# Optimization experiments

Measured on AMD Instinct MI355X. Metric: run time of the kernel, lower is better.

Reference implementation:

```python
import jax, jax.numpy as jnp
import numpy as np

N = 100000      # nodes
E = 1600000     # edges
F_IN = 256      # input feature dim
H = 2           # num heads
D = 64          # hidden per head (H*D = 128)
C = 64          # output classes
N_TRAIN = 10000
SLOPE = 0.2     # DGL GATConv leaky_relu negative slope
BN_EPS = 1e-5


def setup_inputs() -> dict:
    key = jax.random.key(0)
    ks = jax.random.split(key, 20)
    sc = lambda k, shape, fan: jax.random.normal(k, shape, jnp.float32) * np.float32(1.0 / np.sqrt(fan))
    inp = {}
    inp["feature"] = jax.random.normal(ks[0], (N, F_IN), jnp.float32)
    inp["label"] = jax.random.randint(ks[1], (N,), 0, C, dtype=jnp.int32)
    inp["train_nodes"] = jax.random.randint(ks[2], (N_TRAIN,), 0, N, dtype=jnp.int32)
    inp["src"] = jax.random.randint(ks[3], (E,), 0, N, dtype=jnp.int32)
    inp["dst"] = jax.random.randint(ks[4], (E,), 0, N, dtype=jnp.int32)
    # GATConv layer 0: F_IN -> H*D
    inp["W0"] = sc(ks[5], (F_IN, H * D), F_IN)
    inp["al0"] = sc(ks[6], (H, D), D)
    inp["ar0"] = sc(ks[7], (H, D), D)
    inp["b0"] = jnp.zeros((H * D,), jnp.float32)
    # GATConv layer 1: H*D -> H*D
    inp["W1"] = sc(ks[8], (H * D, H * D), H * D)
    inp["al1"] = sc(ks[9], (H, D), D)
    inp["ar1"] = sc(ks[10], (H, D), D)
    inp["b1"] = jnp.zeros((H * D,), jnp.float32)
    # dense head: Linear(H*D -> D) + ReLU, Linear(D -> C), BatchNorm1d(C)
    inp["Wout"] = sc(ks[11], (H * D, D), H * D)
    inp["bout"] = jnp.zeros((D,), jnp.float32)
    inp["Wfc"] = sc(ks[12], (D, C), D)
    inp["bfc"] = jnp.zeros((C,), jnp.float32)
    inp["gamma"] = jnp.ones((C,), jnp.float32)
    inp["beta"] = jnp.zeros((C,), jnp.float32)
    return inp


def gat_conv(x, W, al, ar, b, src, dst):
    """DGL-style GATConv: gather, edge attention, segment softmax over dst, scatter-sum, ReLU."""
    n = x.shape[0]
    feat = (x @ W).reshape(n, H, D)                      # [N,H,D]
    el = jnp.einsum('nhd,hd->nh', feat, al)              # src attention term
    er = jnp.einsum('nhd,hd->nh', feat, ar)              # dst attention term
    e = jax.nn.leaky_relu(el[src] + er[dst], SLOPE)      # [E,H]
    m = jax.ops.segment_max(e, dst, num_segments=n)      # per-dst max for stable softmax
    exp_e = jnp.exp(e - m[dst])
    denom = jax.ops.segment_sum(exp_e, dst, num_segments=n)
    alpha = exp_e / jnp.maximum(denom[dst], 1e-16)       # [E,H]
    msg = feat[src] * alpha[:, :, None]                  # [E,H,D]
    out = jax.ops.segment_sum(msg, dst, num_segments=n)  # [N,H,D]
    out = out + b.reshape(1, H, D)
    return jax.nn.relu(out)


def reference(feature, label, train_nodes, src, dst,
              W0, al0, ar0, b0, W1, al1, ar1, b1,
              Wout, bout, Wfc, bfc, gamma, beta):
    h = gat_conv(feature, W0, al0, ar0, b0, src, dst).reshape(N, H * D)
    h = gat_conv(h, W1, al1, ar1, b1, src, dst).reshape(N, H * D)
    h = jax.nn.relu(h @ Wout + bout)
    h = h @ Wfc + bfc
    # BatchNorm1d in training mode: batch statistics (biased variance)
    mu = jnp.mean(h, axis=0)
    var = jnp.mean((h - mu) ** 2, axis=0)
    h = (h - mu) * jax.lax.rsqrt(var + BN_EPS) * gamma + beta
    p = jax.nn.softmax(h, axis=1)
    # F.cross_entropy applied to softmax outputs, exactly as in the source
    sel = p[train_nodes]                                  # [N_TRAIN, C]
    logp = jax.nn.log_softmax(sel, axis=1)
    lab = label[train_nodes]
    loss = -jnp.mean(jnp.take_along_axis(logp, lab[:, None], axis=1))
    return (p, loss)
```

## Files before the change

kernel.cpp:

```cpp
#include <hip/hip_runtime.h>

#define SLOPE 0.2f
#define BN_EPS 1e-5f

#define CSR_TILE 4096
#define NBUCK_SH 9
#define BCAP 16384

typedef __attribute__((ext_vector_type(8))) short bf16x8;
typedef __attribute__((ext_vector_type(4))) float f32x4;

__device__ __forceinline__ float wave_sum(float v){
  #pragma unroll
  for(int o=32;o;o>>=1) v += __shfl_xor(v,o);
  return v;
}
__device__ __forceinline__ float wave_max(float v){
  #pragma unroll
  for(int o=32;o;o>>=1) v = fmaxf(v,__shfl_xor(v,o));
  return v;
}
__device__ __forceinline__ unsigned pack_bf16(float a, float b){
  unsigned ua=__float_as_uint(a), ub=__float_as_uint(b);
  ua += 0x7fffu + ((ua>>16)&1u);
  ub += 0x7fffu + ((ub>>16)&1u);
  return (ua>>16) | (ub & 0xffff0000u);
}
__device__ __forceinline__ float bf_lo(unsigned u){ return __uint_as_float(u<<16); }
__device__ __forceinline__ float bf_hi(unsigned u){ return __uint_as_float(u & 0xffff0000u); }

__global__ __launch_bounds__(256) void wtrans2(const float* __restrict__ W0,
    const float* __restrict__ W1, unsigned* __restrict__ Wt0, unsigned* __restrict__ Wt1){
  int idx = blockIdx.x*256 + threadIdx.x;
  if(blockIdx.x < 64){
    int c = idx >> 7, kp = idx & 127;
    Wt0[(size_t)c*128 + kp] = pack_bf16(W0[(size_t)(2*kp)*128 + c], W0[(size_t)(2*kp+1)*128 + c]);
  } else {
    int i2 = idx - 64*256;
    int c = i2 >> 6, kp = i2 & 63;
    Wt1[(size_t)c*64 + kp] = pack_bf16(W1[(size_t)(2*kp)*128 + c], W1[(size_t)(2*kp+1)*128 + c]);
  }
}

template<int AF32>
__global__ __launch_bounds__(256) void gemm_mfma(const void* __restrict__ Aptr,
    const unsigned* __restrict__ Wt, unsigned* __restrict__ outb,
    const float* __restrict__ al, const float* __restrict__ ar,
    float* __restrict__ el, float* __restrict__ er, int n, int K){
  __shared__ unsigned sA[128][36];
  int t = threadIdx.x;
  int w = t >> 6, l = t & 63;
  int wr = (w >> 1) * 64, wc = (w & 1) * 64;
  int row0 = blockIdx.x * 128;
  int K2 = K >> 1;
  int ktiles = K >> 6;

  int srow[4], sslot[4];
  #pragma unroll
  for(int i=0;i<4;i++){ int u4 = t + i*256; srow[i] = u4>>3; sslot[i] = u4&7; }

  uint4 pa[4][2];

  auto load_tile = [&](int kt){
    if(AF32){
      const float* A = (const float*)Aptr;
      #pragma unroll
      for(int i=0;i<4;i++){
        int gr = row0 + srow[i];
        pa[i][0] = make_uint4(0,0,0,0);
        pa[i][1] = make_uint4(0,0,0,0);
        if(gr < n){
          const unsigned* ap = (const unsigned*)(A + (size_t)gr*K + kt*64 + sslot[i]*8);
          pa[i][0] = *(const uint4*)ap;
          pa[i][1] = *(const uint4*)(ap+4);
        }
      }
    } else {
      const unsigned* A = (const unsigned*)Aptr;
      #pragma unroll
      for(int i=0;i<4;i++){
        int gr = row0 + srow[i];
        pa[i][0] = make_uint4(0,0,0,0);
        if(gr < n) pa[i][0] = *(const uint4*)(A + (size_t)gr*K2 + kt*32 + sslot[i]*4);
      }
    }
  };

  auto store_tile = [&](){
    if(AF32){
      #pragma unroll
      for(int i=0;i<4;i++){
        uint4 v;
        v.x = pack_bf16(__uint_as_float(pa[i][0].x), __uint_as_float(pa[i][0].y));
        v.y = pack_bf16(__uint_as_float(pa[i][0].z), __uint_as_float(pa[i][0].w));
        v.z = pack_bf16(__uint_as_float(pa[i][1].x), __uint_as_float(pa[i][1].y));
        v.w = pack_bf16(__uint_as_float(pa[i][1].z), __uint_as_float(pa[i][1].w));
        *(uint4*)&sA[srow[i]][sslot[i]*4] = v;
      }
    } else {
      #pragma unroll
      for(int i=0;i<4;i++)
        *(uint4*)&sA[srow[i]][sslot[i]*4] = pa[i][0];
    }
  };

  f32x4 zero4 = {0.f,0.f,0.f,0.f};
  f32x4 acc[4][4];
  #pragma unroll
  for(int i=0;i<4;i++)
    #pragma unroll
    for(int j=0;j<4;j++) acc[i][j] = zero4;

  int rl = l & 15;
  load_tile(0);
  for(int kt = 0; kt < ktiles; ++kt){
    store_tile();
    __syncthreads();
    if(kt+1 < ktiles) load_tile(kt+1);
    #pragma unroll
    for(int ks=0; ks<2; ++ks){
      int koff = ks*16 + (l>>4)*4;
      bf16x8 a[4], b[4];
      #pragma unroll
      for(int f=0; f<4; f++)
        b[f] = *(const bf16x8*)&Wt[(size_t)(wc + f*16 + rl)*K2 + kt*32 + koff];
      #pragma unroll
      for(int f=0; f<4; f++)
        a[f] = *(const bf16x8*)&sA[wr + f*16 + rl][koff];
      #pragma unroll
      for(int i=0;i<4;i++)
        #pragma unroll
        for(int j=0;j<4;j++)
          acc[i][j] = __builtin_amdgcn_mfma_f32_16x16x32_bf16(a[i], b[j], acc[i][j], 0, 0, 0);
    }
    __syncthreads();
  }

  #pragma unroll
  for(int i=0;i<4;i++){
    #pragma unroll
    for(int j=0;j<4;j++){
      #pragma unroll
      for(int g=0;g<4;g++){
        float v  = acc[i][j][g];
        float vp = __shfl_xor(v, 1);
        if(!(l & 1)){
          unsigned pv = pack_bf16(v, vp);
          int grow = row0 + wr + i*16 + (l>>4)*4 + g;
          int gcol = wc + j*16 + (l&15);
          if(grow < n) outb[(size_t)grow*64 + (gcol>>1)] = pv;
        }
      }
    }
  }

  {
    int h = wc >> 6;
    float alv[4], arv[4];
    #pragma unroll
    for(int j=0;j<4;j++){
      int c = wc + j*16 + (l&15);
      alv[j] = al[c]; arv[j] = ar[c];
    }
    #pragma unroll
    for(int i=0;i<4;i++){
      #pragma unroll
      for(int g=0;g<4;g++){
        float pe = acc[i][0][g]*alv[0] + acc[i][1][g]*alv[1]
                 + acc[i][2][g]*alv[2] + acc[i][3][g]*alv[3];
        float qe = acc[i][0][g]*arv[0] + acc[i][1][g]*arv[1]
                 + acc[i][2][g]*arv[2] + acc[i][3][g]*arv[3];
        #pragma unroll
        for(int o=8;o;o>>=1){ pe += __shfl_xor(pe,o); qe += __shfl_xor(qe,o); }
        if((l & 15) == 0){
          int grow = row0 + wr + i*16 + (l>>4)*4 + g;
          if(grow < n){
            el[(size_t)grow*2 + h] = pe;
            er[(size_t)grow*2 + h] = qe;
          }
        }
      }
    }
  }
}

__global__ __launch_bounds__(256) void csrABC(const int* __restrict__ src,
    const int* __restrict__ dst, int* __restrict__ cursor,
    unsigned* __restrict__ tmp, int E, int nbuck){
  __shared__ unsigned eb[CSR_TILE];
  __shared__ short    ebb[CSR_TILE];
  __shared__ int hist[256];
  __shared__ int basel[256];
  int t = threadIdx.x;
  hist[t] = 0;
  __syncthreads();
  int base = blockIdx.x * CSR_TILE;
  int cnt  = min(CSR_TILE, E - base);
  for(int k = t; k < cnt; k += 256){
    int d = dst[base + k];
    int s = src[base + k];
    int b = d >> NBUCK_SH;
    eb[k]  = (unsigned)s | ((unsigned)(d & ((1<<NBUCK_SH)-1)) << 17);
    ebb[k] = (short)b;
    atomicAdd(&hist[b], 1);
  }
  __syncthreads();
  if(t < nbuck && hist[t] > 0)
    basel[t] = atomicAdd(&cursor[t], hist[t]);
  __syncthreads();
  hist[t] = 0;
  __syncthreads();
  for(int k = t; k < cnt; k += 256){
    int b = ebb[k];
    int r = atomicAdd(&hist[b], 1);
    tmp[(size_t)b*BCAP + basel[b] + r] = eb[k];
  }
}

__global__ __launch_bounds__(256) void scanB(const int* __restrict__ cursor,
    int* __restrict__ bbase, int nbuck, int E){
  __shared__ int ls[256];
  int t = threadIdx.x;
  int v = (t < nbuck) ? cursor[t] : 0;
  ls[t] = v; __syncthreads();
  for(int o=1;o<256;o<<=1){
    int x = (t>=o) ? ls[t-o] : 0;
    __syncthreads();
    ls[t] += x;
    __syncthreads();
  }
  if(t < nbuck) bbase[t] = ls[t] - v;
  if(t == 0) bbase[nbuck] = E;
}

__global__ __launch_bounds__(512) void csrD(const unsigned* __restrict__ tmp,
    const int* __restrict__ bbase, int* __restrict__ rowptr,
    int* __restrict__ esrc, int N, int E, int nbuck){
  __shared__ int hist[512];
  __shared__ int ls[512];
  int t = threadIdx.x;
  int b = blockIdx.x;
  int base = bbase[b];
  int cnt  = bbase[b+1] - base;
  const unsigned* tp = tmp + (size_t)b*BCAP;
  int n0   = b << NBUCK_SH;
  int nn   = min(512, N - n0);
  hist[t] = 0;
  __syncthreads();
  for(int i = t; i < cnt; i += 512)
    atomicAdd(&hist[tp[i] >> 17], 1);
  __syncthreads();
  int v = hist[t];
  ls[t] = v; __syncthreads();
  for(int o=1;o<512;o<<=1){
    int x = (t>=o) ? ls[t-o] : 0;
    __syncthreads();
    ls[t] += x;
    __syncthreads();
  }
  int rp = ls[t] - v;
  if(t < nn) rowptr[n0 + t] = base + rp;
  if(b == nbuck-1 && t == 0) rowptr[N] = E;
  __syncthreads();
  hist[t] = rp;
  __syncthreads();
  for(int i = t; i < cnt; i += 512){
    unsigned v2 = tp[i];
    int dl = v2 >> 17;
    int s  = v2 & 0x1FFFF;
    int r  = atomicAdd(&hist[dl], 1);
    esrc[base + r] = s;
  }
}

__device__ __forceinline__ void agg_chunk(const unsigned* __restrict__ featb,
    int s, unsigned wp, int nval, int lane, int shamt, float& acc0, float& acc1){
  for(int e = 0; e < nval; e += 8){
    unsigned v[8]; float w[8];
    #pragma unroll
    for(int u=0;u<8;u++){
      int se       = __shfl(s,  e+u);
      unsigned wpe = __shfl(wp, e+u);
      w[u] = __uint_as_float((wpe << shamt) & 0xffff0000u);
      v[u] = featb[((unsigned)se << 6) + (unsigned)lane];
    }
    #pragma unroll
    for(int u=0;u<8;u++){
      acc0 += bf_lo(v[u]) * w[u];
      acc1 += bf_hi(v[u]) * w[u];
    }
  }
}

__global__ __launch_bounds__(256) void agg_kernel(const unsigned* __restrict__ featb,
    const float* __restrict__ el, const float* __restrict__ er,
    const int* __restrict__ rowptr, const int* __restrict__ esrc,
    const float* __restrict__ bias, unsigned* __restrict__ outp, int n){
  int wid = (blockIdx.x*blockDim.x + threadIdx.x) >> 6;
  int lane = threadIdx.x & 63;
  if(wid >= n) return;
  int beg = rowptr[wid], end = rowptr[wid+1];
  int deg = end - beg;
  float2 erd = *(const float2*)&er[(size_t)wid*2];
  int shamt = (lane < 32) ? 16 : 0;
  float acc0 = 0.f, acc1 = 0.f;

  if(deg <= 64){
    int s = (lane < deg) ? esrc[beg + lane] : 0;
    float2 elv = *(const float2*)&el[(size_t)s*2];
    float e0 = elv.x + erd.x, e1 = elv.y + erd.y;
    e0 = (e0 >= 0.f) ? e0 : SLOPE*e0;
    e1 = (e1 >= 0.f) ? e1 : SLOPE*e1;
    float p0 = __expf(e0), p1 = __expf(e1);
    if(lane >= deg){ p0 = 0.f; p1 = 0.f; }
    float d0 = wave_sum(p0), d1 = wave_sum(p1);
    unsigned wp = pack_bf16(p0 / fmaxf(d0, 1e-16f), p1 / fmaxf(d1, 1e-16f));
    agg_chunk(featb, s, wp, deg, lane, shamt, acc0, acc1);
  } else {
    float d0 = 0.f, d1 = 0.f;
    for(int base = beg; base < end; base += 64){
      int idx = base + lane;
      int s = (idx < end) ? esrc[idx] : 0;
      float2 elv = *(const float2*)&el[(size_t)s*2];
      float e0 = elv.x + erd.x, e1 = elv.y + erd.y;
      e0 = (e0 >= 0.f) ? e0 : SLOPE*e0;
      e1 = (e1 >= 0.f) ? e1 : SLOPE*e1;
      float p0 = __expf(e0), p1 = __expf(e1);
      if(idx >= end){ p0 = 0.f; p1 = 0.f; }
      d0 += p0; d1 += p1;
    }
    d0 = wave_sum(d0); d1 = wave_sum(d1);
    float inv0 = 1.0f / fmaxf(d0, 1e-16f);
    float inv1 = 1.0f / fmaxf(d1, 1e-16f);
    for(int base = beg; base < end; base += 64){
      int idx = base + lane;
      int s = (idx < end) ? esrc[idx] : 0;
      float2 elv = *(const float2*)&el[(size_t)s*2];
      float e0 = elv.x + erd.x, e1 = elv.y + erd.y;
      e0 = (e0 >= 0.f) ? e0 : SLOPE*e0;
      e1 = (e1 >= 0.f) ? e1 : SLOPE*e1;
      unsigned wp = pack_bf16(__expf(e0) * inv0, __expf(e1) * inv1);
      if(idx >= end) wp = 0;
      agg_chunk(featb, s, wp, min(64, end - base), lane, shamt, acc0, acc1);
    }
  }
  float2 bb = *(const float2*)&bias[2*lane];
  outp[(size_t)wid*64 + lane] =
      pack_bf16(fmaxf(acc0 + bb.x, 0.f), fmaxf(acc1 + bb.y, 0.f));
}

__global__ __launch_bounds__(256) void head_kernel(const unsigned* __restrict__ h,
    const float* __restrict__ Wout, const float* __restrict__ bout,
    const float* __restrict__ Wfc, const float* __restrict__ bfc,
    float* __restrict__ hfc, int n){
  __shared__ float sAT[32][68];
  __shared__ float sWo[32][68];
  __shared__ float sOT[64][68];
  __shared__ float sF [64][68];
  int t = threadIdx.x;
  int cx = t & 15;
  int ry = t >> 4;
  int row0 = blockIdx.x * 64;

  {
    int kr = t >> 4;
    int c0 = (t & 15) * 4;
    #pragma unroll
    for(int i=0;i<4;i++)
      *(float4*)&sF[kr+i*16][c0] = *(const float4*)&Wfc[(size_t)(kr+i*16)*64 + c0];
  }

  float acc[4][4] = {};
  for(int k0 = 0; k0 < 128; k0 += 32){
    #pragma unroll
    for(int u=0;u<2;u++){
      int f4 = t*2 + u;
      int r  = f4 >> 3;
      int kc = (f4 & 7) * 4;
      int gr = row0 + r;
      uint2 v = make_uint2(0,0);
      if(gr < n) v = *(const uint2*)&h[(size_t)gr*64 + ((k0+kc)>>1)];
      sAT[kc+0][r] = bf_lo(v.x);
      sAT[kc+1][r] = bf_hi(v.x);
      sAT[kc+2][r] = bf_lo(v.y);
      sAT[kc+3][r] = bf_hi(v.y);
    }
    #pragma unroll
    for(int u=0;u<2;u++){
      int f4 = t*2 + u;
      int kr = f4 >> 4;
      int c0 = (f4 & 15) * 4;
      *(float4*)&sWo[kr][c0] = *(const float4*)&Wout[(size_t)(k0+kr)*64 + c0];
    }
    __syncthreads();
    #pragma unroll 8
    for(int kk = 0; kk < 32; ++kk){
      float4 a4 = *(const float4*)&sAT[kk][ry*4];
      float4 b4 = *(const float4*)&sWo[kk][cx*4];
      float a[4] = {a4.x,a4.y,a4.z,a4.w};
      float b[4] = {b4.x,b4.y,b4.z,b4.w};
      #pragma unroll
      for(int i=0;i<4;i++)
        #pragma unroll
        for(int j=0;j<4;j++) acc[i][j] += a[i]*b[j];
    }
    __syncthreads();
  }
  {
    float4 bb = *(const float4*)&bout[cx*4];
    float bv[4] = {bb.x,bb.y,bb.z,bb.w};
    #pragma unroll
    for(int i=0;i<4;i++)
      #pragma unroll
      for(int j=0;j<4;j++)
        sOT[cx*4+j][ry*4+i] = fmaxf(acc[i][j] + bv[j], 0.f);
  }
  __syncthreads();
  float acc2[4][4] = {};
  #pragma unroll 8
  for(int kk = 0; kk < 64; ++kk){
    float4 a4 = *(const float4*)&sOT[kk][ry*4];
    float4 b4 = *(const float4*)&sF [kk][cx*4];
    float a[4] = {a4.x,a4.y,a4.z,a4.w};
    float b[4] = {b4.x,b4.y,b4.z,b4.w};
    #pragma unroll
    for(int i=0;i<4;i++)
      #pragma unroll
      for(int j=0;j<4;j++) acc2[i][j] += a[i]*b[j];
  }
  {
    float4 bb = *(const float4*)&bfc[cx*4];
    #pragma unroll
    for(int i=0;i<4;i++){
      int gr = row0 + ry*4 + i;
      if(gr < n){
        float4 o = make_float4(acc2[i][0]+bb.x, acc2[i][1]+bb.y,
                               acc2[i][2]+bb.z, acc2[i][3]+bb.w);
        *(float4*)&hfc[(size_t)gr*64 + cx*4] = o;
      }
    }
  }
}

__global__ __launch_bounds__(256) void bn_stats(const float* __restrict__ hfc,
    float* __restrict__ psum, float* __restrict__ psum2, int n){
  int t = threadIdx.x; int c = t & 63; int g = t >> 6;
  int rpb = (n + gridDim.x - 1) / gridDim.x;
  int r0 = blockIdx.x * rpb;
  int r1 = min(n, r0 + rpb);
  float s = 0.f, s2 = 0.f;
  for(int r = r0 + g; r < r1; r += 4){
    float v = hfc[(size_t)r*64 + c];
    s += v; s2 += v*v;
  }
  __shared__ float ls[256], ls2[256];
  ls[t]=s; ls2[t]=s2; __syncthreads();
  if(t < 64){
    s  = ls[t]+ls[t+64]+ls[t+128]+ls[t+192];
    s2 = ls2[t]+ls2[t+64]+ls2[t+128]+ls2[t+192];
    psum[blockIdx.x*64 + t]  = s;
    psum2[blockIdx.x*64 + t] = s2;
  }
}

__global__ __launch_bounds__(64) void bn_fin(const float* __restrict__ psum,
    const float* __restrict__ psum2, const float* __restrict__ gamma,
    const float* __restrict__ beta, float* __restrict__ scsh, int n, int nb){
  int c = threadIdx.x;
  float s=0.f, s2=0.f;
  for(int b=0;b<nb;b++){ s += psum[b*64+c]; s2 += psum2[b*64+c]; }
  float mu  = s / n;
  float var = s2 / n - mu*mu;
  float scale = rsqrtf(var + BN_EPS) * gamma[c];
  scsh[c]    = scale;
  scsh[64+c] = beta[c] - mu*scale;
}

__global__ __launch_bounds__(256) void bn_softmax(const float* __restrict__ hfc,
    const float* __restrict__ scsh, float* __restrict__ p, int n){
  int wid = (blockIdx.x*blockDim.x + threadIdx.x) >> 6;
  int lane = threadIdx.x & 63;
  if(wid >= n) return;
  float y = hfc[(size_t)wid*64 + lane]*scsh[lane] + scsh[64+lane];
  float m = wave_max(y);
  float e = expf(y - m);
  float s = wave_sum(e);
  p[(size_t)wid*64 + lane] = e / s;
}

__global__ __launch_bounds__(256) void loss1(const float* __restrict__ p,
    const int* __restrict__ train, const int* __restrict__ label,
    float* __restrict__ part, int ntrain){
  int lane = threadIdx.x & 63; int w = threadIdx.x >> 6;
  int gw = blockIdx.x*4 + w; int nw = gridDim.x*4;
  float acc = 0.f;
  for(int t = gw; t < ntrain; t += nw){
    int node = train[t];
    float v = p[(size_t)node*64 + lane];
    float m = wave_max(v);
    float e = expf(v - m);
    float s = wave_sum(e);
    float logp = (v - m) - logf(s);
    int lab = label[node];
    if(lane == lab) acc += logp;
  }
  acc = wave_sum(acc);
  __shared__ float ls[4];
  if(lane == 0) ls[w] = acc;
  __syncthreads();
  if(threadIdx.x == 0) part[blockIdx.x] = ls[0]+ls[1]+ls[2]+ls[3];
}

__global__ void loss2(const float* __restrict__ part, float* __restrict__ out,
                      int nb, int ntrain){
  if(threadIdx.x == 0){
    float s = 0.f;
    for(int i=0;i<nb;i++) s += part[i];
    out[0] = -s / (float)ntrain;
  }
}

extern "C" void kernel_launch(void* const* d_in, const int* in_sizes, int n_in,
                              void* d_out, int out_size, void* d_ws, size_t ws_size,
                              hipStream_t stream){
  const float* feature = (const float*)d_in[0];
  const int*   label   = (const int*)d_in[1];
  const int*   train   = (const int*)d_in[2];
  const int*   src     = (const int*)d_in[3];
  const int*   dst     = (const int*)d_in[4];
  const float* W0   = (const float*)d_in[5];
  const float* al0  = (const float*)d_in[6];
  const float* ar0  = (const float*)d_in[7];
  const float* b0   = (const float*)d_in[8];
  const float* W1   = (const float*)d_in[9];
  const float* al1  = (const float*)d_in[10];
  const float* ar1  = (const float*)d_in[11];
  const float* b1   = (const float*)d_in[12];
  const float* Wout = (const float*)d_in[13];
  const float* bout = (const float*)d_in[14];
  const float* Wfc  = (const float*)d_in[15];
  const float* bfc  = (const float*)d_in[16];
  const float* gamma= (const float*)d_in[17];
  const float* beta = (const float*)d_in[18];

  const int N  = in_sizes[1];
  const int NT = in_sizes[2];
  const int E  = in_sizes[3];

  const int nbuck  = (N + (1<<NBUCK_SH) - 1) >> NBUCK_SH;
  const int ntiles = (E + CSR_TILE - 1) / CSR_TILE;

  size_t off = 0;
  auto alloc = [&](size_t bytes)->void*{
    void* pp = (char*)d_ws + off;
    off += (bytes + 255) & ~(size_t)255;
    return pp;
  };
  unsigned* featb16 = (unsigned*)alloc((size_t)N*64*4);
  unsigned* hbuf2   = (unsigned*)alloc((size_t)N*64*4);
  float* el      = (float*)alloc((size_t)N*2*4);
  float* er      = (float*)alloc((size_t)N*2*4);
  int*   rowptr  = (int*)alloc((size_t)(N+1)*4);
  int*   esrc    = (int*)alloc((size_t)E*4);
  int*   cursor  = (int*)alloc((size_t)256*4);
  int*   bbase   = (int*)alloc((size_t)(nbuck+1)*4);
  unsigned* Wt0  = (unsigned*)alloc((size_t)128*128*4);
  unsigned* Wt1  = (unsigned*)alloc((size_t)128*64*4);
  float* psum    = (float*)alloc((size_t)256*64*4);
  float* psum2   = (float*)alloc((size_t)256*64*4);
  float* scsh    = (float*)alloc(128*4);
  float* lpart   = (float*)alloc(256*4);
  float* hfc     = (float*)featb16;
  unsigned* tmp  = hbuf2;

  float* p_out   = (float*)d_out;
  float* loss_out= (float*)d_out + (size_t)N*64;

  const int nwaveblk = (N + 3) / 4;

  wtrans2<<<96, 256, 0, stream>>>(W0, W1, Wt0, Wt1);

  hipMemsetAsync(cursor, 0, 256*4, stream);
  csrABC<<<ntiles, 256, 0, stream>>>(src, dst, cursor, tmp, E, nbuck);
  scanB<<<1, 256, 0, stream>>>(cursor, bbase, nbuck, E);
  csrD<<<nbuck, 512, 0, stream>>>(tmp, bbase, rowptr, esrc, N, E, nbuck);

  gemm_mfma<1><<<(N+127)/128, 256, 0, stream>>>(feature, Wt0, featb16, al0, ar0, el, er, N, 256);
  agg_kernel<<<nwaveblk, 256, 0, stream>>>(featb16, el, er, rowptr, esrc, b0, hbuf2, N);

  gemm_mfma<0><<<(N+127)/128, 256, 0, stream>>>(hbuf2, Wt1, featb16, al1, ar1, el, er, N, 128);
  agg_kernel<<<nwaveblk, 256, 0, stream>>>(featb16, el, er, rowptr, esrc, b1, hbuf2, N);

  head_kernel<<<(N+63)/64, 256, 0, stream>>>(hbuf2, Wout, bout, Wfc, bfc, hfc, N);

  bn_stats<<<256, 256, 0, stream>>>(hfc, psum, psum2, N);
  bn_fin<<<1, 64, 0, stream>>>(psum, psum2, gamma, beta, scsh, N, 256);
  bn_softmax<<<nwaveblk, 256, 0, stream>>>(hfc, scsh, p_out, N);

  loss1<<<40, 256, 0, stream>>>(p_out, train, label, lpart, NT);
  loss2<<<1, 64, 0, stream>>>(lpart, loss_out, 40, NT);
}
```

Baseline: 456.2 us.

## Widen aggregation gathers to 8-byte loads over edge pairs and double-buffer GEMM prefetch

The aggregation inner loop now splits the wave into two halves. Each half processes alternate edges, and each lane loads a uint2 (four bf16 features) instead of one 32-bit word. The halves are combined with a cross-half shuffle before the biased ReLU store. This halves the number of gather instructions per edge row and doubles the bytes each instruction fetches. Separately, the GEMM K dimension becomes a compile-time template parameter, with two register prefetch buffers and a fully unrolled k loop so loads run two tiles ahead. This costs more registers.

```diff
diff --git a/kernel.cpp b/kernel.cpp
--- a/kernel.cpp
+++ b/kernel.cpp
@@ -42,26 +42,26 @@
   }
 }
 
-template<int AF32>
+template<int AF32, int KK>
 __global__ __launch_bounds__(256) void gemm_mfma(const void* __restrict__ Aptr,
     const unsigned* __restrict__ Wt, unsigned* __restrict__ outb,
     const float* __restrict__ al, const float* __restrict__ ar,
-    float* __restrict__ el, float* __restrict__ er, int n, int K){
+    float* __restrict__ el, float* __restrict__ er, int n){
+  constexpr int K2 = KK >> 1;
+  constexpr int KT = KK >> 6;
   __shared__ unsigned sA[128][36];
   int t = threadIdx.x;
   int w = t >> 6, l = t & 63;
   int wr = (w >> 1) * 64, wc = (w & 1) * 64;
   int row0 = blockIdx.x * 128;
-  int K2 = K >> 1;
-  int ktiles = K >> 6;
 
   int srow[4], sslot[4];
   #pragma unroll
   for(int i=0;i<4;i++){ int u4 = t + i*256; srow[i] = u4>>3; sslot[i] = u4&7; }
 
-  uint4 pa[4][2];
-
-  auto load_tile = [&](int kt){
+  uint4 pa0[4][2], pa1[4][2];
+
+  auto load_into = [&](uint4 (&pa)[4][2], int kt){
     if(AF32){
       const float* A = (const float*)Aptr;
       #pragma unroll
@@ -70,7 +70,7 @@
         pa[i][0] = make_uint4(0,0,0,0);
         pa[i][1] = make_uint4(0,0,0,0);
         if(gr < n){
-          const unsigned* ap = (const unsigned*)(A + (size_t)gr*K + kt*64 + sslot[i]*8);
+          const unsigned* ap = (const unsigned*)(A + (size_t)gr*KK + kt*64 + sslot[i]*8);
           pa[i][0] = *(const uint4*)ap;
           pa[i][1] = *(const uint4*)(ap+4);
         }
@@ -86,7 +86,7 @@
     }
   };
 
-  auto store_tile = [&](){
+  auto store_from = [&](uint4 (&pa)[4][2]){
     if(AF32){
       #pragma unroll
       for(int i=0;i<4;i++){
@@ -112,11 +112,15 @@
     for(int j=0;j<4;j++) acc[i][j] = zero4;
 
   int rl = l & 15;
-  load_tile(0);
-  for(int kt = 0; kt < ktiles; ++kt){
-    store_tile();
-    __syncthreads();
-    if(kt+1 < ktiles) load_tile(kt+1);
+  load_into(pa0, 0);
+  if(KT > 1) load_into(pa1, 1);
+  #pragma unroll
+  for(int kt = 0; kt < KT; ++kt){
+    if(kt & 1) store_from(pa1); else store_from(pa0);
+    __syncthreads();
+    if(kt + 2 < KT){
+      if(kt & 1) load_into(pa1, kt+2); else load_into(pa0, kt+2);
+    }
     #pragma unroll
     for(int ks=0; ks<2; ++ks){
       int koff = ks*16 + (l>>4)*4;
@@ -273,21 +277,29 @@
   }
 }
 
-__device__ __forceinline__ void agg_chunk(const unsigned* __restrict__ featb,
-    int s, unsigned wp, int nval, int lane, int shamt, float& acc0, float& acc1){
-  for(int e = 0; e < nval; e += 8){
-    unsigned v[8]; float w[8];
+__device__ __forceinline__ void agg_chunk2(const unsigned* __restrict__ featb,
+    int s, unsigned wp, int nval, int lane,
+    float& a0, float& a1, float& a2, float& a3){
+  int half = lane >> 5;
+  int l31  = lane & 31;
+  int shamt = (l31 < 16) ? 16 : 0;
+  unsigned loff = ((unsigned)l31) << 1;
+  for(int e = 0; e < nval; e += 16){
+    uint2 v[8]; float w[8];
     #pragma unroll
     for(int u=0;u<8;u++){
-      int se       = __shfl(s,  e+u);
-      unsigned wpe = __shfl(wp, e+u);
+      int idx = e + 2*u + half;
+      int se       = __shfl(s,  idx);
+      unsigned wpe = __shfl(wp, idx);
       w[u] = __uint_as_float((wpe << shamt) & 0xffff0000u);
-      v[u] = featb[((unsigned)se << 6) + (unsigned)lane];
+      v[u] = *(const uint2*)(featb + (((unsigned)se) << 6) + loff);
     }
     #pragma unroll
     for(int u=0;u<8;u++){
-      acc0 += bf_lo(v[u]) * w[u];
-      acc1 += bf_hi(v[u]) * w[u];
+      a0 += bf_lo(v[u].x) * w[u];
+      a1 += bf_hi(v[u].x) * w[u];
+      a2 += bf_lo(v[u].y) * w[u];
+      a3 += bf_hi(v[u].y) * w[u];
     }
   }
 }
@@ -302,8 +314,7 @@
   int beg = rowptr[wid], end = rowptr[wid+1];
   int deg = end - beg;
   float2 erd = *(const float2*)&er[(size_t)wid*2];
-  int shamt = (lane < 32) ? 16 : 0;
-  float acc0 = 0.f, acc1 = 0.f;
+  float a0=0.f, a1=0.f, a2=0.f, a3=0.f;
 
   if(deg <= 64){
     int s = (lane < deg) ? esrc[beg + lane] : 0;
@@ -315,7 +326,7 @@
     if(lane >= deg){ p0 = 0.f; p1 = 0.f; }
     float d0 = wave_sum(p0), d1 = wave_sum(p1);
     unsigned wp = pack_bf16(p0 / fmaxf(d0, 1e-16f), p1 / fmaxf(d1, 1e-16f));
-    agg_chunk(featb, s, wp, deg, lane, shamt, acc0, acc1);
+    agg_chunk2(featb, s, wp, deg, lane, a0, a1, a2, a3);
   } else {
     float d0 = 0.f, d1 = 0.f;
     for(int base = beg; base < end; base += 64){
@@ -341,12 +352,20 @@
       e1 = (e1 >= 0.f) ? e1 : SLOPE*e1;
       unsigned wp = pack_bf16(__expf(e0) * inv0, __expf(e1) * inv1);
       if(idx >= end) wp = 0;
-      agg_chunk(featb, s, wp, min(64, end - base), lane, shamt, acc0, acc1);
-    }
-  }
-  float2 bb = *(const float2*)&bias[2*lane];
-  outp[(size_t)wid*64 + lane] =
-      pack_bf16(fmaxf(acc0 + bb.x, 0.f), fmaxf(acc1 + bb.y, 0.f));
+      agg_chunk2(featb, s, wp, min(64, end - base), lane, a0, a1, a2, a3);
+    }
+  }
+  a0 += __shfl_xor(a0, 32);
+  a1 += __shfl_xor(a1, 32);
+  a2 += __shfl_xor(a2, 32);
+  a3 += __shfl_xor(a3, 32);
+  if(lane < 32){
+    float4 bb = *(const float4*)&bias[lane*4];
+    uint2 o;
+    o.x = pack_bf16(fmaxf(a0 + bb.x, 0.f), fmaxf(a1 + bb.y, 0.f));
+    o.y = pack_bf16(fmaxf(a2 + bb.z, 0.f), fmaxf(a3 + bb.w, 0.f));
+    *(uint2*)&outp[(size_t)wid*64 + lane*2] = o;
+  }
 }
 
 __global__ __launch_bounds__(256) void head_kernel(const unsigned* __restrict__ h,
@@ -585,10 +604,10 @@
   scanB<<<1, 256, 0, stream>>>(cursor, bbase, nbuck, E);
   csrD<<<nbuck, 512, 0, stream>>>(tmp, bbase, rowptr, esrc, N, E, nbuck);
 
-  gemm_mfma<1><<<(N+127)/128, 256, 0, stream>>>(feature, Wt0, featb16, al0, ar0, el, er, N, 256);
+  gemm_mfma<1,256><<<(N+127)/128, 256, 0, stream>>>(feature, Wt0, featb16, al0, ar0, el, er, N);
   agg_kernel<<<nwaveblk, 256, 0, stream>>>(featb16, el, er, rowptr, esrc, b0, hbuf2, N);
 
-  gemm_mfma<0><<<(N+127)/128, 256, 0, stream>>>(hbuf2, Wt1, featb16, al1, ar1, el, er, N, 128);
+  gemm_mfma<0,128><<<(N+127)/128, 256, 0, stream>>>(hbuf2, Wt1, featb16, al1, ar1, el, er, N);
   agg_kernel<<<nwaveblk, 256, 0, stream>>>(featb16, el, er, rowptr, esrc, b1, hbuf2, N);
 
   head_kernel<<<(N+63)/64, 256, 0, stream>>>(hbuf2, Wout, bout, Wfc, bfc, hfc, N);
```

Result: no change. 463.8 us (+1.7%).

## Fuse CSR bucketing with layer-0 GEMM and BN stats into head kernel

Applied to the files above, without the earlier changes.

Merges the CSR bucket-scatter kernel and the first GEMM into one launch that splits blocks by index, so the irregular scatter can overlap with the MFMA GEMM. The cursor reset moves into the weight-transpose kernel, and the bucket scan moves into csrD, removing the memset and scanB launches. BatchNorm partial sums are now computed inside head_kernel from shared memory, which drops the separate bn_stats pass over hfc. In exchange, every csrD block redundantly recomputes the prefix scan, and the fused kernel's shared-memory footprint may lower occupancy.

```diff
diff --git a/kernel.cpp b/kernel.cpp
--- a/kernel.cpp
+++ b/kernel.cpp
@@ -30,7 +30,8 @@
 __device__ __forceinline__ float bf_hi(unsigned u){ return __uint_as_float(u & 0xffff0000u); }
 
 __global__ __launch_bounds__(256) void wtrans2(const float* __restrict__ W0,
-    const float* __restrict__ W1, unsigned* __restrict__ Wt0, unsigned* __restrict__ Wt1){
+    const float* __restrict__ W1, unsigned* __restrict__ Wt0, unsigned* __restrict__ Wt1,
+    int* __restrict__ cursor){
   int idx = blockIdx.x*256 + threadIdx.x;
   if(blockIdx.x < 64){
     int c = idx >> 7, kp = idx & 127;
@@ -39,21 +40,58 @@
     int i2 = idx - 64*256;
     int c = i2 >> 6, kp = i2 & 63;
     Wt1[(size_t)c*64 + kp] = pack_bf16(W1[(size_t)(2*kp)*128 + c], W1[(size_t)(2*kp+1)*128 + c]);
-  }
-}
-
-template<int AF32>
-__global__ __launch_bounds__(256) void gemm_mfma(const void* __restrict__ Aptr,
+    if(blockIdx.x == 95) cursor[threadIdx.x] = 0;
+  }
+}
+
+template<int AF32, int KK>
+__global__ __launch_bounds__(256) void fat_kernel(const void* __restrict__ Aptr,
     const unsigned* __restrict__ Wt, unsigned* __restrict__ outb,
     const float* __restrict__ al, const float* __restrict__ ar,
-    float* __restrict__ el, float* __restrict__ er, int n, int K){
-  __shared__ unsigned sA[128][36];
+    float* __restrict__ el, float* __restrict__ er, int n,
+    const int* __restrict__ src, const int* __restrict__ dst,
+    int* __restrict__ cursor, unsigned* __restrict__ tmp, int E, int nbuck, int ncsr){
+  constexpr int K2 = KK >> 1;
+  constexpr int KT = KK >> 6;
+  __shared__ unsigned smem[6656];
   int t = threadIdx.x;
+
+  if((int)blockIdx.x < ncsr){
+    unsigned* eb  = smem;
+    short*    ebb = (short*)(smem + 4096);
+    int*      hist= (int*)(smem + 6144);
+    int*      basel=(int*)(smem + 6400);
+    hist[t] = 0;
+    __syncthreads();
+    int base = blockIdx.x * CSR_TILE;
+    int cnt  = min(CSR_TILE, E - base);
+    for(int k = t; k < cnt; k += 256){
+      int d = dst[base + k];
+      int s = src[base + k];
+      int b = d >> NBUCK_SH;
+      eb[k]  = (unsigned)s | ((unsigned)(d & ((1<<NBUCK_SH)-1)) << 17);
+      ebb[k] = (short)b;
+      atomicAdd(&hist[b], 1);
+    }
+    __syncthreads();
+    if(t < nbuck && hist[t] > 0)
+      basel[t] = atomicAdd(&cursor[t], hist[t]);
+    __syncthreads();
+    hist[t] = 0;
+    __syncthreads();
+    for(int k = t; k < cnt; k += 256){
+      int b = ebb[k];
+      int r = atomicAdd(&hist[b], 1);
+      tmp[(size_t)b*BCAP + basel[b] + r] = eb[k];
+    }
+    return;
+  }
+
+  unsigned (*sA)[36] = (unsigned(*)[36])smem;
+  int bid = blockIdx.x - ncsr;
   int w = t >> 6, l = t & 63;
   int wr = (w >> 1) * 64, wc = (w & 1) * 64;
-  int row0 = blockIdx.x * 128;
-  int K2 = K >> 1;
-  int ktiles = K >> 6;
+  int row0 = bid * 128;
 
   int srow[4], sslot[4];
   #pragma unroll
@@ -70,7 +108,7 @@
         pa[i][0] = make_uint4(0,0,0,0);
         pa[i][1] = make_uint4(0,0,0,0);
         if(gr < n){
-          const unsigned* ap = (const unsigned*)(A + (size_t)gr*K + kt*64 + sslot[i]*8);
+          const unsigned* ap = (const unsigned*)(A + (size_t)gr*KK + kt*64 + sslot[i]*8);
           pa[i][0] = *(const uint4*)ap;
           pa[i][1] = *(const uint4*)(ap+4);
         }
@@ -113,10 +151,11 @@
 
   int rl = l & 15;
   load_tile(0);
-  for(int kt = 0; kt < ktiles; ++kt){
+  #pragma unroll
+  for(int kt = 0; kt < KT; ++kt){
     store_tile();
     __syncthreads();
-    if(kt+1 < ktiles) load_tile(kt+1);
+    if(kt+1 < KT) load_tile(kt+1);
     #pragma unroll
     for(int ks=0; ks<2; ++ks){
       int koff = ks*16 + (l>>4)*4;
@@ -184,67 +223,29 @@
   }
 }
 
-__global__ __launch_bounds__(256) void csrABC(const int* __restrict__ src,
-    const int* __restrict__ dst, int* __restrict__ cursor,
-    unsigned* __restrict__ tmp, int E, int nbuck){
-  __shared__ unsigned eb[CSR_TILE];
-  __shared__ short    ebb[CSR_TILE];
-  __shared__ int hist[256];
-  __shared__ int basel[256];
-  int t = threadIdx.x;
-  hist[t] = 0;
-  __syncthreads();
-  int base = blockIdx.x * CSR_TILE;
-  int cnt  = min(CSR_TILE, E - base);
-  for(int k = t; k < cnt; k += 256){
-    int d = dst[base + k];
-    int s = src[base + k];
-    int b = d >> NBUCK_SH;
-    eb[k]  = (unsigned)s | ((unsigned)(d & ((1<<NBUCK_SH)-1)) << 17);
-    ebb[k] = (short)b;
-    atomicAdd(&hist[b], 1);
-  }
-  __syncthreads();
-  if(t < nbuck && hist[t] > 0)
-    basel[t] = atomicAdd(&cursor[t], hist[t]);
-  __syncthreads();
-  hist[t] = 0;
-  __syncthreads();
-  for(int k = t; k < cnt; k += 256){
-    int b = ebb[k];
-    int r = atomicAdd(&hist[b], 1);
-    tmp[(size_t)b*BCAP + basel[b] + r] = eb[k];
-  }
-}
-
-__global__ __launch_bounds__(256) void scanB(const int* __restrict__ cursor,
-    int* __restrict__ bbase, int nbuck, int E){
-  __shared__ int ls[256];
-  int t = threadIdx.x;
-  int v = (t < nbuck) ? cursor[t] : 0;
-  ls[t] = v; __syncthreads();
-  for(int o=1;o<256;o<<=1){
-    int x = (t>=o) ? ls[t-o] : 0;
-    __syncthreads();
-    ls[t] += x;
-    __syncthreads();
-  }
-  if(t < nbuck) bbase[t] = ls[t] - v;
-  if(t == 0) bbase[nbuck] = E;
-}
-
 __global__ __launch_bounds__(512) void csrD(const unsigned* __restrict__ tmp,
-    const int* __restrict__ bbase, int* __restrict__ rowptr,
+    const int* __restrict__ cursor, int* __restrict__ rowptr,
     int* __restrict__ esrc, int N, int E, int nbuck){
+  __shared__ int sc[256];
   __shared__ int hist[512];
   __shared__ int ls[512];
   int t = threadIdx.x;
   int b = blockIdx.x;
-  int base = bbase[b];
-  int cnt  = bbase[b+1] - base;
+  if(t < 256) sc[t] = (t < nbuck) ? cursor[t] : 0;
+  __syncthreads();
+  for(int o=1;o<256;o<<=1){
+    int x = (t>=o && t<256) ? sc[t-o] : 0;
+    __syncthreads();
+    if(t < 256) sc[t] += x;
+    __syncthreads();
+  }
+  __shared__ int s_base, s_cnt;
+  if(t == 0){ s_cnt = cursor[b]; s_base = sc[b] - s_cnt; }
+  __syncthreads();
+  int base = s_base, cnt = s_cnt;
   const unsigned* tp = tmp + (size_t)b*BCAP;
-  int n0   = b << NBUCK_SH;
-  int nn   = min(512, N - n0);
+  int n0 = b << NBUCK_SH;
+  int nn = min(512, N - n0);
   hist[t] = 0;
   __syncthreads();
   for(int i = t; i < cnt; i += 512)
@@ -352,7 +353,8 @@
 __global__ __launch_bounds__(256) void head_kernel(const unsigned* __restrict__ h,
     const float* __restrict__ Wout, const float* __restrict__ bout,
     const float* __restrict__ Wfc, const float* __restrict__ bfc,
-    float* __restrict__ hfc, int n){
+    float* __restrict__ hfc, float* __restrict__ psum, float* __restrict__ psum2,
+    int n){
   __shared__ float sAT[32][68];
   __shared__ float sWo[32][68];
   __shared__ float sOT[64][68];
@@ -428,52 +430,63 @@
       #pragma unroll
       for(int j=0;j<4;j++) acc2[i][j] += a[i]*b[j];
   }
+  __syncthreads();
   {
     float4 bb = *(const float4*)&bfc[cx*4];
+    float bv[4] = {bb.x,bb.y,bb.z,bb.w};
     #pragma unroll
     for(int i=0;i<4;i++){
       int gr = row0 + ry*4 + i;
+      float o0 = acc2[i][0]+bv[0], o1 = acc2[i][1]+bv[1];
+      float o2 = acc2[i][2]+bv[2], o3 = acc2[i][3]+bv[3];
       if(gr < n){
-        float4 o = make_float4(acc2[i][0]+bb.x, acc2[i][1]+bb.y,
-                               acc2[i][2]+bb.z, acc2[i][3]+bb.w);
-        *(float4*)&hfc[(size_t)gr*64 + cx*4] = o;
+        *(float4*)&hfc[(size_t)gr*64 + cx*4] = make_float4(o0,o1,o2,o3);
+        sOT[ry*4+i][cx*4+0] = o0;
+        sOT[ry*4+i][cx*4+1] = o1;
+        sOT[ry*4+i][cx*4+2] = o2;
+        sOT[ry*4+i][cx*4+3] = o3;
+      } else {
+        sOT[ry*4+i][cx*4+0] = 0.f;
+        sOT[ry*4+i][cx*4+1] = 0.f;
+        sOT[ry*4+i][cx*4+2] = 0.f;
+        sOT[ry*4+i][cx*4+3] = 0.f;
       }
     }
   }
-}
-
-__global__ __launch_bounds__(256) void bn_stats(const float* __restrict__ hfc,
-    float* __restrict__ psum, float* __restrict__ psum2, int n){
+  __syncthreads();
+  if(t < 64){
+    float s = 0.f, s2 = 0.f;
+    #pragma unroll 8
+    for(int r = 0; r < 64; ++r){
+      float v = sOT[r][t];
+      s += v; s2 += v*v;
+    }
+    psum [(size_t)blockIdx.x*64 + t] = s;
+    psum2[(size_t)blockIdx.x*64 + t] = s2;
+  }
+}
+
+__global__ __launch_bounds__(256) void bn_fin(const float* __restrict__ psum,
+    const float* __restrict__ psum2, const float* __restrict__ gamma,
+    const float* __restrict__ beta, float* __restrict__ scsh, int n, int nb){
+  __shared__ float ls[256], ls2[256];
   int t = threadIdx.x; int c = t & 63; int g = t >> 6;
-  int rpb = (n + gridDim.x - 1) / gridDim.x;
-  int r0 = blockIdx.x * rpb;
-  int r1 = min(n, r0 + rpb);
   float s = 0.f, s2 = 0.f;
-  for(int r = r0 + g; r < r1; r += 4){
-    float v = hfc[(size_t)r*64 + c];
-    s += v; s2 += v*v;
-  }
-  __shared__ float ls[256], ls2[256];
-  ls[t]=s; ls2[t]=s2; __syncthreads();
+  for(int b = g; b < nb; b += 4){
+    s  += psum [(size_t)b*64 + c];
+    s2 += psum2[(size_t)b*64 + c];
+  }
+  ls[t] = s; ls2[t] = s2;
+  __syncthreads();
   if(t < 64){
     s  = ls[t]+ls[t+64]+ls[t+128]+ls[t+192];
     s2 = ls2[t]+ls2[t+64]+ls2[t+128]+ls2[t+192];
-    psum[blockIdx.x*64 + t]  = s;
-    psum2[blockIdx.x*64 + t] = s2;
-  }
-}
-
-__global__ __launch_bounds__(64) void bn_fin(const float* __restrict__ psum,
-    const float* __restrict__ psum2, const float* __restrict__ gamma,
-    const float* __restrict__ beta, float* __restrict__ scsh, int n, int nb){
-  int c = threadIdx.x;
-  float s=0.f, s2=0.f;
-  for(int b=0;b<nb;b++){ s += psum[b*64+c]; s2 += psum2[b*64+c]; }
-  float mu  = s / n;
-  float var = s2 / n - mu*mu;
-  float scale = rsqrtf(var + BN_EPS) * gamma[c];
-  scsh[c]    = scale;
-  scsh[64+c] = beta[c] - mu*scale;
+    float mu  = s / n;
+    float var = s2 / n - mu*mu;
+    float scale = rsqrtf(var + BN_EPS) * gamma[t];
+    scsh[t]    = scale;
+    scsh[64+t] = beta[t] - mu*scale;
+  }
 }
 
 __global__ __launch_bounds__(256) void bn_softmax(const float* __restrict__ hfc,
@@ -549,6 +562,8 @@
 
   const int nbuck  = (N + (1<<NBUCK_SH) - 1) >> NBUCK_SH;
   const int ntiles = (E + CSR_TILE - 1) / CSR_TILE;
+  const int ngemm  = (N + 127) / 128;
+  const int nhead  = (N + 63) / 64;
 
   size_t off = 0;
   auto alloc = [&](size_t bytes)->void*{
@@ -563,11 +578,10 @@
   int*   rowptr  = (int*)alloc((size_t)(N+1)*4);
   int*   esrc    = (int*)alloc((size_t)E*4);
   int*   cursor  = (int*)alloc((size_t)256*4);
-  int*   bbase   = (int*)alloc((size_t)(nbuck+1)*4);
   unsigned* Wt0  = (unsigned*)alloc((size_t)128*128*4);
   unsigned* Wt1  = (unsigned*)alloc((size_t)128*64*4);
-  float* psum    = (float*)alloc((size_t)256*64*4);
-  float* psum2   = (float*)alloc((size_t)256*64*4);
+  float* psum    = (float*)alloc((size_t)(nhead+1)*64*4);
+  float* psum2   = (float*)alloc((size_t)(nhead+1)*64*4);
   float* scsh    = (float*)alloc(128*4);
   float* lpart   = (float*)alloc(256*4);
   float* hfc     = (float*)featb16;
@@ -578,23 +592,24 @@
 
   const int nwaveblk = (N + 3) / 4;
 
-  wtrans2<<<96, 256, 0, stream>>>(W0, W1, Wt0, Wt1);
-
-  hipMemsetAsync(cursor, 0, 256*4, stream);
-  csrABC<<<ntiles, 256, 0, stream>>>(src, dst, cursor, tmp, E, nbuck);
-  scanB<<<1, 256, 0, stream>>>(cursor, bbase, nbuck, E);
-  csrD<<<nbuck, 512, 0, stream>>>(tmp, bbase, rowptr, esrc, N, E, nbuck);
-
-  gemm_mfma<1><<<(N+127)/128, 256, 0, stream>>>(feature, Wt0, featb16, al0, ar0, el, er, N, 256);
+  wtrans2<<<96, 256, 0, stream>>>(W0, W1, Wt0, Wt1, cursor);
+
+  fat_kernel<1,256><<<ntiles + ngemm, 256, 0, stream>>>(feature, Wt0, featb16,
+      al0, ar0, el, er, N, src, dst, cursor, tmp, E, nbuck, ntiles);
+
+  csrD<<<nbuck, 512, 0, stream>>>(tmp, cursor, rowptr, esrc, N, E, nbuck);
+
   agg_kernel<<<nwaveblk, 256, 0, stream>>>(featb16, el, er, rowptr, esrc, b0, hbuf2, N);
 
-  gemm_mfma<0><<<(N+127)/128, 256, 0, stream>>>(hbuf2, Wt1, featb16, al1, ar1, el, er, N, 128);
+  fat_kernel<0,128><<<ngemm, 256, 0, stream>>>(hbuf2, Wt1, featb16,
+      al1, ar1, el, er, N, src, dst, cursor, tmp, E, nbuck, 0);
+
   agg_kernel<<<nwaveblk, 256, 0, stream>>>(featb16, el, er, rowptr, esrc, b1, hbuf2, N);
 
-  head_kernel<<<(N+63)/64, 256, 0, stream>>>(hbuf2, Wout, bout, Wfc, bfc, hfc, N);
-
-  bn_stats<<<256, 256, 0, stream>>>(hfc, psum, psum2, N);
-  bn_fin<<<1, 64, 0, stream>>>(psum, psum2, gamma, beta, scsh, N, 256);
+  head_kernel<<<nhead, 256, 0, stream>>>(hbuf2, Wout, bout, Wfc, bfc, hfc, psum, psum2, N);
+
+  bn_fin<<<1, 256, 0, stream>>>(psum, psum2, gamma, beta, scsh, N, nhead);
+
   bn_softmax<<<nwaveblk, 256, 0, stream>>>(hfc, scsh, p_out, N);
 
   loss1<<<40, 256, 0, stream>>>(p_out, train, label, lpart, NT);
```

Result: no change. 465.3 us (+2.0%).
